# Performance work log

Measured on AMD Instinct MI355X. Metric: run time of the kernel, lower is better.

## Reference

```python
import jax, jax.numpy as jnp
import numpy as np

N_NODES = 50000
N_EDGES = 500000
IN_DIM = 128
HIDDEN = 32
HEADS = 8
OUT_DIM = HIDDEN * HEADS  # 256
NEG_SLOPE = 0.2


def setup_inputs() -> dict:
    key = jax.random.key(0)
    ks = jax.random.split(key, 10)
    s = lambda fan: 1.0 / np.sqrt(fan)
    x = jax.random.normal(ks[0], (N_NODES, IN_DIM), dtype=jnp.float32)
    edge_index = jax.random.randint(ks[1], (2, N_EDGES), 0, N_NODES, dtype=jnp.int32)
    W1 = jax.random.normal(ks[2], (IN_DIM, HEADS * HIDDEN), jnp.float32) * s(IN_DIM)
    a_src1 = jax.random.normal(ks[3], (HEADS, HIDDEN), jnp.float32) * s(HIDDEN)
    a_dst1 = jax.random.normal(ks[4], (HEADS, HIDDEN), jnp.float32) * s(HIDDEN)
    b1 = jnp.zeros((HEADS * HIDDEN,), jnp.float32)
    W2 = jax.random.normal(ks[5], (OUT_DIM, OUT_DIM), jnp.float32) * s(OUT_DIM)
    a_src2 = jax.random.normal(ks[6], (1, OUT_DIM), jnp.float32) * s(OUT_DIM)
    a_dst2 = jax.random.normal(ks[7], (1, OUT_DIM), jnp.float32) * s(OUT_DIM)
    b2 = jnp.zeros((OUT_DIM,), jnp.float32)
    return {"x": x, "edge_index": edge_index, "W1": W1, "a_src1": a_src1,
            "a_dst1": a_dst1, "b1": b1, "W2": W2, "a_src2": a_src2,
            "a_dst2": a_dst2, "b2": b2}


def _gat_layer(x, src, dst, W, a_src, a_dst, b, heads, ch, concat):
    N = x.shape[0]
    h = (x @ W).reshape(N, heads, ch)                      # [N,H,C]
    e_src = jnp.sum(h * a_src[None], axis=-1)              # [N,H]
    e_dst = jnp.sum(h * a_dst[None], axis=-1)              # [N,H]
    e = jax.nn.leaky_relu(e_src[src] + e_dst[dst], NEG_SLOPE)  # [E,H]
    # softmax over incoming edges of each destination node
    m = jax.ops.segment_max(e, dst, num_segments=N)        # [N,H]
    e = jnp.exp(e - m[dst])
    denom = jax.ops.segment_sum(e, dst, num_segments=N)    # [N,H]
    alpha = e / (denom[dst] + 1e-16)                       # [E,H]
    msg = h[src] * alpha[:, :, None]                       # [E,H,C]
    out = jax.ops.segment_sum(msg, dst, num_segments=N)    # [N,H,C]
    out = out.reshape(N, heads * ch) if concat else out.mean(axis=1)
    return out + b


def reference(x, edge_index, W1, a_src1, a_dst1, b1, W2, a_src2, a_dst2, b2):
    N = x.shape[0]
    # add self loops (PyG GATConv default)
    loops = jnp.arange(N, dtype=edge_index.dtype)
    src = jnp.concatenate([edge_index[0], loops])
    dst = jnp.concatenate([edge_index[1], loops])
    # dropout is identity in eval mode
    h = _gat_layer(x, src, dst, W1, a_src1, a_dst1, b1, HEADS, HIDDEN, True)
    h = jax.nn.elu(h)
    out = _gat_layer(h, src, dst, W2, a_src2, a_dst2, b2, 1, OUT_DIM, False)
    return out
```

## Files before the change

kernel.cpp:

```cpp
#include <hip/hip_runtime.h>
#include <math.h>

#define N_NODES 50000
#define E_ORIG  500000
#define E_TOT   550000
#define NB      196

typedef _Float16 half8 __attribute__((ext_vector_type(8)));
typedef _Float16 half4 __attribute__((ext_vector_type(4)));
typedef float    v4f   __attribute__((ext_vector_type(4)));

__global__ void k_prepw(const float* __restrict__ W1, const float* __restrict__ W2,
                        const float* __restrict__ as2, const float* __restrict__ ad2,
                        const int* __restrict__ ei,
                        _Float16* __restrict__ w1t, _Float16* __restrict__ w2t,
                        float* __restrict__ vs2, float* __restrict__ vd2,
                        int* __restrict__ deg) {
    int i = blockIdx.x * blockDim.x + threadIdx.x;
    if (i < E_TOT) {
        int d = (i < E_ORIG) ? ei[E_ORIG + i] : (i - E_ORIG);
        atomicAdd(&deg[d], 1);
        return;
    }
    int j = i - E_TOT;
    if (j < 128 * 256) {
        int k = j >> 8, c = j & 255;
        w1t[(size_t)c * 128 + k] = (_Float16)W1[j];
        return;
    }
    j -= 128 * 256;
    if (j < 256 * 256) {
        int k = j >> 8, c = j & 255;
        w2t[(size_t)c * 256 + k] = (_Float16)W2[j];
        return;
    }
    j -= 256 * 256;
    if (j < 256) {
        float s = 0.f, d = 0.f;
        for (int c = 0; c < 256; c++) {
            float w = W2[(size_t)j * 256 + c];
            s += w * as2[c];
            d += w * ad2[c];
        }
        vs2[j] = s;
        vd2[j] = d;
    }
}

__global__ __launch_bounds__(256) void k_blocksum(const int* __restrict__ deg,
                                                  int* __restrict__ bsum) {
    int t = threadIdx.x;
    int i = blockIdx.x * 256 + t;
    int v = (i < N_NODES) ? deg[i] : 0;
#pragma unroll
    for (int mk = 1; mk < 64; mk <<= 1) v += __shfl_xor(v, mk, 64);
    __shared__ int ws[4];
    if ((t & 63) == 0) ws[t >> 6] = v;
    __syncthreads();
    if (t == 0) bsum[blockIdx.x] = ws[0] + ws[1] + ws[2] + ws[3];
}

__global__ __launch_bounds__(256) void k_scanbsum(const int* __restrict__ bsum,
                                                  int* __restrict__ boff) {
    __shared__ int s[256];
    int t = threadIdx.x;
    int v = (t < NB) ? bsum[t] : 0;
    s[t] = v;
    __syncthreads();
    for (int o = 1; o < 256; o <<= 1) {
        int x = (t >= o) ? s[t - o] : 0;
        __syncthreads();
        s[t] += x;
        __syncthreads();
    }
    if (t <= NB) boff[t] = (t == 0) ? 0 : s[t - 1];
}

__global__ __launch_bounds__(256) void k_offsets(const int* __restrict__ deg,
                                                 const int* __restrict__ boff,
                                                 int* __restrict__ offsets,
                                                 int* __restrict__ cur) {
    __shared__ int s[256];
    int t = threadIdx.x;
    int i = blockIdx.x * 256 + t;
    int v = (i < N_NODES) ? deg[i] : 0;
    s[t] = v;
    __syncthreads();
    for (int o = 1; o < 256; o <<= 1) {
        int x = (t >= o) ? s[t - o] : 0;
        __syncthreads();
        s[t] += x;
        __syncthreads();
    }
    int off = boff[blockIdx.x] + s[t] - v;
    if (i <= N_NODES) {
        offsets[i] = off;
        if (i < N_NODES) cur[i] = off;
    }
}

__global__ void k_scatter(const int* __restrict__ ei, int* __restrict__ cur,
                          int* __restrict__ csr_src) {
    int e = blockIdx.x * blockDim.x + threadIdx.x;
    if (e >= E_TOT) return;
    int s, d;
    if (e < E_ORIG) { s = ei[e]; d = ei[E_ORIG + e]; }
    else            { s = e - E_ORIG; d = s; }
    int slot = atomicAdd(&cur[d], 1);
    csr_src[slot] = s;
}

__global__ __launch_bounds__(256) void k_gemm1(
    const float* __restrict__ X, const _Float16* __restrict__ Bt,
    const float* __restrict__ a_s, const float* __restrict__ a_d,
    _Float16* __restrict__ H, float* __restrict__ es, float* __restrict__ ed) {
    int t = threadIdx.x, w = t >> 6, lane = t & 63;
    int quad = lane >> 4, l16 = lane & 15;
    int row0 = blockIdx.x * 32;
    int colbase = w * 64;

    v4f acc[2][4];
#pragma unroll
    for (int i = 0; i < 2; i++)
#pragma unroll
        for (int j = 0; j < 4; j++) acc[i][j] = (v4f){0.f, 0.f, 0.f, 0.f};

    int r0 = row0 + l16;      if (r0 >= N_NODES) r0 = N_NODES - 1;
    int r1 = row0 + 16 + l16; if (r1 >= N_NODES) r1 = N_NODES - 1;
    const float4* a0p = (const float4*)(X + (size_t)r0 * 128) + quad * 2;
    const float4* a1p = (const float4*)(X + (size_t)r1 * 128) + quad * 2;
    const half8* bp[4];
#pragma unroll
    for (int ct = 0; ct < 4; ct++)
        bp[ct] = (const half8*)(Bt + (size_t)(colbase + ct * 16 + l16) * 128 + quad * 8);

#pragma unroll
    for (int kc = 0; kc < 4; kc++) {
        float4 f0 = a0p[kc * 8], f1 = a0p[kc * 8 + 1];
        float4 f2 = a1p[kc * 8], f3 = a1p[kc * 8 + 1];
        half8 av0 = (half8){(_Float16)f0.x, (_Float16)f0.y, (_Float16)f0.z, (_Float16)f0.w,
                            (_Float16)f1.x, (_Float16)f1.y, (_Float16)f1.z, (_Float16)f1.w};
        half8 av1 = (half8){(_Float16)f2.x, (_Float16)f2.y, (_Float16)f2.z, (_Float16)f2.w,
                            (_Float16)f3.x, (_Float16)f3.y, (_Float16)f3.z, (_Float16)f3.w};
#pragma unroll
        for (int ct = 0; ct < 4; ct++) {
            half8 bv = bp[ct][kc * 4];
            acc[0][ct] = __builtin_amdgcn_mfma_f32_16x16x32_f16(av0, bv, acc[0][ct], 0, 0, 0);
            acc[1][ct] = __builtin_amdgcn_mfma_f32_16x16x32_f16(av1, bv, acc[1][ct], 0, 0, 0);
        }
    }

    float asv[4], adv[4];
#pragma unroll
    for (int ct = 0; ct < 4; ct++) {
        asv[ct] = a_s[colbase + ct * 16 + l16];
        adv[ct] = a_d[colbase + ct * 16 + l16];
    }
#pragma unroll
    for (int rt = 0; rt < 2; rt++) {
#pragma unroll
        for (int hp = 0; hp < 2; hp++) {
#pragma unroll
            for (int reg = 0; reg < 4; reg++) {
                float ps = acc[rt][2 * hp][reg] * asv[2 * hp] +
                           acc[rt][2 * hp + 1][reg] * asv[2 * hp + 1];
                float pd = acc[rt][2 * hp][reg] * adv[2 * hp] +
                           acc[rt][2 * hp + 1][reg] * adv[2 * hp + 1];
#pragma unroll
                for (int mk = 1; mk < 16; mk <<= 1) {
                    ps += __shfl_xor(ps, mk, 64);
                    pd += __shfl_xor(pd, mk, 64);
                }
                if (l16 == 0) {
                    int row = row0 + rt * 16 + quad * 4 + reg;
                    if (row < N_NODES) {
                        int head = w * 2 + hp;
                        es[(size_t)row * 8 + head] = ps;
                        ed[(size_t)row * 8 + head] = pd;
                    }
                }
            }
        }
    }

    __shared__ _Float16 SH[16][264];
#pragma unroll
    for (int rt = 0; rt < 2; rt++) {
        if (rt) __syncthreads();
#pragma unroll
        for (int ct = 0; ct < 4; ct++)
#pragma unroll
            for (int reg = 0; reg < 4; reg++)
                SH[quad * 4 + reg][colbase + ct * 16 + l16] = (_Float16)acc[rt][ct][reg];
        __syncthreads();
#pragma unroll
        for (int j = 0; j < 2; j++) {
            int c = j * 256 + t;
            int row = c >> 5, col8 = c & 31;
            int gr = row0 + rt * 16 + row;
            if (gr < N_NODES)
                *(half8*)(H + (size_t)gr * 256 + col8 * 8) = *(const half8*)&SH[row][col8 * 8];
        }
    }
}

__global__ __launch_bounds__(256) void k_gemm2(
    const _Float16* __restrict__ A, const _Float16* __restrict__ Bt,
    const float* __restrict__ bias, float* __restrict__ OUT) {
    int t = threadIdx.x, w = t >> 6, lane = t & 63;
    int quad = lane >> 4, l16 = lane & 15;
    int row0 = blockIdx.x * 32;
    int colbase = w * 64;

    v4f acc[2][4];
#pragma unroll
    for (int i = 0; i < 2; i++)
#pragma unroll
        for (int j = 0; j < 4; j++) acc[i][j] = (v4f){0.f, 0.f, 0.f, 0.f};

    int r0 = row0 + l16;      if (r0 >= N_NODES) r0 = N_NODES - 1;
    int r1 = row0 + 16 + l16; if (r1 >= N_NODES) r1 = N_NODES - 1;
    const half8* a0 = (const half8*)(A + (size_t)r0 * 256 + quad * 8);
    const half8* a1 = (const half8*)(A + (size_t)r1 * 256 + quad * 8);
    const half8* bp[4];
#pragma unroll
    for (int ct = 0; ct < 4; ct++)
        bp[ct] = (const half8*)(Bt + (size_t)(colbase + ct * 16 + l16) * 256 + quad * 8);

#pragma unroll
    for (int kc = 0; kc < 8; kc++) {
        half8 av0 = a0[kc * 4];
        half8 av1 = a1[kc * 4];
#pragma unroll
        for (int ct = 0; ct < 4; ct++) {
            half8 bv = bp[ct][kc * 4];
            acc[0][ct] = __builtin_amdgcn_mfma_f32_16x16x32_f16(av0, bv, acc[0][ct], 0, 0, 0);
            acc[1][ct] = __builtin_amdgcn_mfma_f32_16x16x32_f16(av1, bv, acc[1][ct], 0, 0, 0);
        }
    }

    __shared__ float SF[16][260];
#pragma unroll
    for (int rt = 0; rt < 2; rt++) {
        if (rt) __syncthreads();
#pragma unroll
        for (int ct = 0; ct < 4; ct++)
#pragma unroll
            for (int reg = 0; reg < 4; reg++)
                SF[quad * 4 + reg][colbase + ct * 16 + l16] = acc[rt][ct][reg];
        __syncthreads();
#pragma unroll
        for (int j = 0; j < 4; j++) {
            int c = j * 256 + t;
            int row = c >> 6, c4 = c & 63;
            int gr = row0 + rt * 16 + row;
            if (gr < N_NODES) {
                float4 v = *(const float4*)&SF[row][c4 * 4];
                float4 bb = ((const float4*)bias)[c4];
                float4 o = make_float4(v.x + bb.x, v.y + bb.y, v.z + bb.z, v.w + bb.w);
                *(float4*)(OUT + (size_t)gr * 256 + c4 * 4) = o;
            }
        }
    }
}

#define EDGE1(I) {                                                         \
    unsigned su = (unsigned)__builtin_amdgcn_readlane(sreg, (I));          \
    float wb = wrow[(I)];                                                  \
    half4 hv = *((const half4*)((const char*)H1 + ((size_t)su << 9)) + lane); \
    a0 += wb * (float)hv[0]; a1 += wb * (float)hv[1];                      \
    a2 += wb * (float)hv[2]; a3 += wb * (float)hv[3];                      \
    den += wb; }

__global__ __launch_bounds__(256) void k_agg1(
    const _Float16* __restrict__ H1, const float* __restrict__ es,
    const float* __restrict__ ed, const int* __restrict__ offsets,
    const int* __restrict__ csr_src, const float* __restrict__ b1,
    const float* __restrict__ vs2, const float* __restrict__ vd2,
    _Float16* __restrict__ out1, float* __restrict__ es2,
    float* __restrict__ ed2) {
    int t = threadIdx.x, w = t >> 6, lane = t & 63;
    int n = blockIdx.x * 4 + w;
    int hB = lane >> 3;
    int beg = offsets[n];
    int deg = offsets[n + 1] - beg;

    float edv[8];
    {
        const float4* edp = (const float4*)(ed + (size_t)n * 8);
        float4 d0 = edp[0], d1 = edp[1];
        edv[0] = d0.x; edv[1] = d0.y; edv[2] = d0.z; edv[3] = d0.w;
        edv[4] = d1.x; edv[5] = d1.y; edv[6] = d1.z; edv[7] = d1.w;
    }

    __shared__ float WT[4][8][68];
    float* wrow = &WT[w][hB][0];

    float a0 = 0.f, a1 = 0.f, a2 = 0.f, a3 = 0.f, den = 0.f;

    for (int base = 0; base < deg; base += 64) {
        int rem = deg - base; if (rem > 64) rem = 64;
        int idx = beg + base + lane;
        if (idx >= E_TOT) idx = E_TOT - 1;
        int sreg = csr_src[idx];

        {
            const float4* ep = (const float4*)(es + ((size_t)(unsigned)sreg << 3));
            float4 e0 = ep[0], e1 = ep[1];
            float l0 = e0.x + edv[0], l1 = e0.y + edv[1];
            float l2 = e0.z + edv[2], l3 = e0.w + edv[3];
            float l4 = e1.x + edv[4], l5 = e1.y + edv[5];
            float l6 = e1.z + edv[6], l7 = e1.w + edv[7];
            l0 = fmaxf(l0, 0.2f * l0); l1 = fmaxf(l1, 0.2f * l1);
            l2 = fmaxf(l2, 0.2f * l2); l3 = fmaxf(l3, 0.2f * l3);
            l4 = fmaxf(l4, 0.2f * l4); l5 = fmaxf(l5, 0.2f * l5);
            l6 = fmaxf(l6, 0.2f * l6); l7 = fmaxf(l7, 0.2f * l7);
            WT[w][0][lane] = __expf(l0); WT[w][1][lane] = __expf(l1);
            WT[w][2][lane] = __expf(l2); WT[w][3][lane] = __expf(l3);
            WT[w][4][lane] = __expf(l4); WT[w][5][lane] = __expf(l5);
            WT[w][6][lane] = __expf(l6); WT[w][7][lane] = __expf(l7);
        }
        asm volatile("s_waitcnt lgkmcnt(0)" ::: "memory");

        int i = 0, nf = rem & ~7;
        for (; i < nf; i += 8) {
            EDGE1(i);     EDGE1(i + 1); EDGE1(i + 2); EDGE1(i + 3);
            EDGE1(i + 4); EDGE1(i + 5); EDGE1(i + 6); EDGE1(i + 7);
        }
        if (rem & 4) { EDGE1(i); EDGE1(i + 1); EDGE1(i + 2); EDGE1(i + 3); i += 4; }
        if (rem & 2) { EDGE1(i); EDGE1(i + 1); i += 2; }
        if (rem & 1) { EDGE1(i); }
    }

    float r = 1.f / (den + 1e-16f);
    float4 bb = ((const float4*)b1)[lane];
    float o0 = a0 * r + bb.x, o1 = a1 * r + bb.y;
    float o2 = a2 * r + bb.z, o3 = a3 * r + bb.w;
    o0 = o0 > 0.f ? o0 : __expf(o0) - 1.f;
    o1 = o1 > 0.f ? o1 : __expf(o1) - 1.f;
    o2 = o2 > 0.f ? o2 : __expf(o2) - 1.f;
    o3 = o3 > 0.f ? o3 : __expf(o3) - 1.f;
    ((half4*)(out1 + (size_t)n * 256))[lane] =
        (half4){(_Float16)o0, (_Float16)o1, (_Float16)o2, (_Float16)o3};

    float4 vs = ((const float4*)vs2)[lane];
    float4 vd = ((const float4*)vd2)[lane];
    float ps = o0 * vs.x + o1 * vs.y + o2 * vs.z + o3 * vs.w;
    float pd = o0 * vd.x + o1 * vd.y + o2 * vd.z + o3 * vd.w;
#pragma unroll
    for (int mk = 1; mk < 64; mk <<= 1) {
        ps += __shfl_xor(ps, mk, 64);
        pd += __shfl_xor(pd, mk, 64);
    }
    if (lane == 0) { es2[n] = ps; ed2[n] = pd; }
}

#define EDGE2(I) {                                                         \
    unsigned su = (unsigned)__builtin_amdgcn_readlane(sreg, (I));          \
    float wb = __int_as_float(__builtin_amdgcn_readlane(wbits, (I)));      \
    half4 hv = *((const half4*)((const char*)O1 + ((size_t)su << 9)) + lane); \
    a0 += wb * (float)hv[0]; a1 += wb * (float)hv[1];                      \
    a2 += wb * (float)hv[2]; a3 += wb * (float)hv[3];                      \
    den += wb; }

__global__ __launch_bounds__(256) void k_agg2(
    const _Float16* __restrict__ O1, const float* __restrict__ es2,
    const float* __restrict__ ed2, const int* __restrict__ offsets,
    const int* __restrict__ csr_src, _Float16* __restrict__ xagg) {
    int t = threadIdx.x, w = t >> 6, lane = t & 63;
    int n = blockIdx.x * 4 + w;
    int beg = offsets[n];
    int deg = offsets[n + 1] - beg;
    float edn = ed2[n];

    float a0 = 0.f, a1 = 0.f, a2 = 0.f, a3 = 0.f, den = 0.f;

    for (int base = 0; base < deg; base += 64) {
        int rem = deg - base; if (rem > 64) rem = 64;
        int idx = beg + base + lane;
        if (idx >= E_TOT) idx = E_TOT - 1;
        int sreg = csr_src[idx];

        float l = es2[sreg] + edn;
        l = fmaxf(l, 0.2f * l);
        int wbits = __float_as_int(__expf(l));

        int i = 0, nf = rem & ~7;
        for (; i < nf; i += 8) {
            EDGE2(i);     EDGE2(i + 1); EDGE2(i + 2); EDGE2(i + 3);
            EDGE2(i + 4); EDGE2(i + 5); EDGE2(i + 6); EDGE2(i + 7);
        }
        if (rem & 4) { EDGE2(i); EDGE2(i + 1); EDGE2(i + 2); EDGE2(i + 3); i += 4; }
        if (rem & 2) { EDGE2(i); EDGE2(i + 1); i += 2; }
        if (rem & 1) { EDGE2(i); }
    }

    float r = 1.f / (den + 1e-16f);
    ((half4*)(xagg + (size_t)n * 256))[lane] =
        (half4){(_Float16)(a0 * r), (_Float16)(a1 * r),
                (_Float16)(a2 * r), (_Float16)(a3 * r)};
}

extern "C" void kernel_launch(void* const* d_in, const int* in_sizes, int n_in,
                              void* d_out, int out_size, void* d_ws, size_t ws_size,
                              hipStream_t stream) {
    const float* x   = (const float*)d_in[0];
    const int*   ei  = (const int*)d_in[1];
    const float* W1  = (const float*)d_in[2];
    const float* as1 = (const float*)d_in[3];
    const float* ad1 = (const float*)d_in[4];
    const float* b1  = (const float*)d_in[5];
    const float* W2  = (const float*)d_in[6];
    const float* as2 = (const float*)d_in[7];
    const float* ad2 = (const float*)d_in[8];
    const float* b2  = (const float*)d_in[9];
    float* out = (float*)d_out;

    char* ws = (char*)d_ws;
    size_t off = 0;
    auto alloc = [&](size_t bytes) {
        void* p = ws + off;
        off = (off + bytes + 255) & ~(size_t)255;
        return p;
    };
    _Float16* h1h     = (_Float16*)alloc((size_t)N_NODES * 256 * 2);
    _Float16* out1h   = (_Float16*)alloc((size_t)N_NODES * 256 * 2);
    _Float16* xagg    = (_Float16*)alloc((size_t)N_NODES * 256 * 2);
    _Float16* w1t     = (_Float16*)alloc((size_t)128 * 256 * 2);
    _Float16* w2t     = (_Float16*)alloc((size_t)256 * 256 * 2);
    float*    es1     = (float*)alloc((size_t)N_NODES * 8 * 4);
    float*    ed1     = (float*)alloc((size_t)N_NODES * 8 * 4);
    float*    es2     = (float*)alloc((size_t)N_NODES * 4);
    float*    ed2     = (float*)alloc((size_t)N_NODES * 4);
    float*    vs2     = (float*)alloc(256 * 4);
    float*    vd2     = (float*)alloc(256 * 4);
    int*      deg     = (int*)alloc((size_t)N_NODES * 4);
    int*      offsets = (int*)alloc((size_t)(N_NODES + 1) * 4);
    int*      cur     = (int*)alloc((size_t)N_NODES * 4);
    int*      csr_src = (int*)alloc((size_t)E_TOT * 4);
    int*      bsum    = (int*)alloc((size_t)NB * 4);
    int*      boff    = (int*)alloc((size_t)(NB + 1) * 4);

    const int TB = 256;
    int gridE = (E_TOT + TB - 1) / TB;
    int gridG = (N_NODES + 31) / 32;
    int gridA = N_NODES / 4;

    hipMemsetAsync(deg, 0, (size_t)N_NODES * 4, stream);
    int prepN = E_TOT + 128 * 256 + 256 * 256 + 256;
    k_prepw<<<(prepN + TB - 1) / TB, TB, 0, stream>>>(W1, W2, as2, ad2, ei,
                                                      w1t, w2t, vs2, vd2, deg);
    k_blocksum<<<NB, TB, 0, stream>>>(deg, bsum);
    k_scanbsum<<<1, TB, 0, stream>>>(bsum, boff);
    k_offsets<<<NB, TB, 0, stream>>>(deg, boff, offsets, cur);
    k_scatter<<<gridE, TB, 0, stream>>>(ei, cur, csr_src);

    k_gemm1<<<gridG, TB, 0, stream>>>(x, w1t, as1, ad1, h1h, es1, ed1);
    k_agg1<<<gridA, TB, 0, stream>>>(h1h, es1, ed1, offsets, csr_src, b1,
                                     vs2, vd2, out1h, es2, ed2);

    k_agg2<<<gridA, TB, 0, stream>>>(out1h, es2, ed2, offsets, csr_src, xagg);
    k_gemm2<<<gridG, TB, 0, stream>>>(xagg, w2t, b2, out);
}
```

Before: 327.8 us.

## Store features head-major and aggregate per head with edge-parallel lanes

H1, es/ed, and out1 now use a head-major layout, so each aggregation block works on one head's 32-channel slice. The slice per node is 64 bytes, meant to keep the gathered working set per head cache-resident. Inside a wave, 8 edges are processed in parallel, each by 4 lanes loading half8, and the partial sums are reduced with shuffles. The layer-2 attention logits are now built with atomicAdd across heads, which needs extra memsets and gives up deterministic float summation order. Agg2 reads O1 per head but still writes xagg row-major.

```diff
diff --git a/kernel.cpp b/kernel.cpp
--- a/kernel.cpp
+++ b/kernel.cpp
@@ -5,6 +5,7 @@
 #define E_ORIG  500000
 #define E_TOT   550000
 #define NB      196
+#define AGG_G   1568
 
 typedef _Float16 half8 __attribute__((ext_vector_type(8)));
 typedef _Float16 half4 __attribute__((ext_vector_type(4)));
@@ -175,8 +176,8 @@
                     int row = row0 + rt * 16 + quad * 4 + reg;
                     if (row < N_NODES) {
                         int head = w * 2 + hp;
-                        es[(size_t)row * 8 + head] = ps;
-                        ed[(size_t)row * 8 + head] = pd;
+                        es[(size_t)head * N_NODES + row] = ps;
+                        ed[(size_t)head * N_NODES + row] = pd;
                     }
                 }
             }
@@ -198,8 +199,11 @@
             int c = j * 256 + t;
             int row = c >> 5, col8 = c & 31;
             int gr = row0 + rt * 16 + row;
-            if (gr < N_NODES)
-                *(half8*)(H + (size_t)gr * 256 + col8 * 8) = *(const half8*)&SH[row][col8 * 8];
+            if (gr < N_NODES) {
+                int head = col8 >> 2, sub = col8 & 3;
+                *(half8*)(H + ((size_t)head * N_NODES + gr) * 32 + sub * 8) =
+                    *(const half8*)&SH[row][col8 * 8];
+            }
         }
     }
 }
@@ -264,141 +268,130 @@
     }
 }
 
-#define EDGE1(I) {                                                         \
-    unsigned su = (unsigned)__builtin_amdgcn_readlane(sreg, (I));          \
-    float wb = wrow[(I)];                                                  \
-    half4 hv = *((const half4*)((const char*)H1 + ((size_t)su << 9)) + lane); \
-    a0 += wb * (float)hv[0]; a1 += wb * (float)hv[1];                      \
-    a2 += wb * (float)hv[2]; a3 += wb * (float)hv[3];                      \
-    den += wb; }
-
 __global__ __launch_bounds__(256) void k_agg1(
-    const _Float16* __restrict__ H1, const float* __restrict__ es,
-    const float* __restrict__ ed, const int* __restrict__ offsets,
+    const _Float16* __restrict__ Hs, const float* __restrict__ esh,
+    const float* __restrict__ edh, const int* __restrict__ offsets,
     const int* __restrict__ csr_src, const float* __restrict__ b1,
     const float* __restrict__ vs2, const float* __restrict__ vd2,
-    _Float16* __restrict__ out1, float* __restrict__ es2,
+    _Float16* __restrict__ out1s, float* __restrict__ es2,
     float* __restrict__ ed2) {
     int t = threadIdx.x, w = t >> 6, lane = t & 63;
-    int n = blockIdx.x * 4 + w;
-    int hB = lane >> 3;
-    int beg = offsets[n];
-    int deg = offsets[n + 1] - beg;
-
-    float edv[8];
-    {
-        const float4* edp = (const float4*)(ed + (size_t)n * 8);
-        float4 d0 = edp[0], d1 = edp[1];
-        edv[0] = d0.x; edv[1] = d0.y; edv[2] = d0.z; edv[3] = d0.w;
-        edv[4] = d1.x; edv[5] = d1.y; edv[6] = d1.z; edv[7] = d1.w;
-    }
-
-    __shared__ float WT[4][8][68];
-    float* wrow = &WT[w][hB][0];
-
-    float a0 = 0.f, a1 = 0.f, a2 = 0.f, a3 = 0.f, den = 0.f;
-
-    for (int base = 0; base < deg; base += 64) {
-        int rem = deg - base; if (rem > 64) rem = 64;
-        int idx = beg + base + lane;
-        if (idx >= E_TOT) idx = E_TOT - 1;
-        int sreg = csr_src[idx];
-
-        {
-            const float4* ep = (const float4*)(es + ((size_t)(unsigned)sreg << 3));
-            float4 e0 = ep[0], e1 = ep[1];
-            float l0 = e0.x + edv[0], l1 = e0.y + edv[1];
-            float l2 = e0.z + edv[2], l3 = e0.w + edv[3];
-            float l4 = e1.x + edv[4], l5 = e1.y + edv[5];
-            float l6 = e1.z + edv[6], l7 = e1.w + edv[7];
-            l0 = fmaxf(l0, 0.2f * l0); l1 = fmaxf(l1, 0.2f * l1);
-            l2 = fmaxf(l2, 0.2f * l2); l3 = fmaxf(l3, 0.2f * l3);
-            l4 = fmaxf(l4, 0.2f * l4); l5 = fmaxf(l5, 0.2f * l5);
-            l6 = fmaxf(l6, 0.2f * l6); l7 = fmaxf(l7, 0.2f * l7);
-            WT[w][0][lane] = __expf(l0); WT[w][1][lane] = __expf(l1);
-            WT[w][2][lane] = __expf(l2); WT[w][3][lane] = __expf(l3);
-            WT[w][4][lane] = __expf(l4); WT[w][5][lane] = __expf(l5);
-            WT[w][6][lane] = __expf(l6); WT[w][7][lane] = __expf(l7);
-        }
-        asm volatile("s_waitcnt lgkmcnt(0)" ::: "memory");
-
-        int i = 0, nf = rem & ~7;
-        for (; i < nf; i += 8) {
-            EDGE1(i);     EDGE1(i + 1); EDGE1(i + 2); EDGE1(i + 3);
-            EDGE1(i + 4); EDGE1(i + 5); EDGE1(i + 6); EDGE1(i + 7);
-        }
-        if (rem & 4) { EDGE1(i); EDGE1(i + 1); EDGE1(i + 2); EDGE1(i + 3); i += 4; }
-        if (rem & 2) { EDGE1(i); EDGE1(i + 1); i += 2; }
-        if (rem & 1) { EDGE1(i); }
-    }
-
-    float r = 1.f / (den + 1e-16f);
-    float4 bb = ((const float4*)b1)[lane];
-    float o0 = a0 * r + bb.x, o1 = a1 * r + bb.y;
-    float o2 = a2 * r + bb.z, o3 = a3 * r + bb.w;
-    o0 = o0 > 0.f ? o0 : __expf(o0) - 1.f;
-    o1 = o1 > 0.f ? o1 : __expf(o1) - 1.f;
-    o2 = o2 > 0.f ? o2 : __expf(o2) - 1.f;
-    o3 = o3 > 0.f ? o3 : __expf(o3) - 1.f;
-    ((half4*)(out1 + (size_t)n * 256))[lane] =
-        (half4){(_Float16)o0, (_Float16)o1, (_Float16)o2, (_Float16)o3};
-
-    float4 vs = ((const float4*)vs2)[lane];
-    float4 vd = ((const float4*)vd2)[lane];
-    float ps = o0 * vs.x + o1 * vs.y + o2 * vs.z + o3 * vs.w;
-    float pd = o0 * vd.x + o1 * vd.y + o2 * vd.z + o3 * vd.w;
-#pragma unroll
-    for (int mk = 1; mk < 64; mk <<= 1) {
-        ps += __shfl_xor(ps, mk, 64);
-        pd += __shfl_xor(pd, mk, 64);
-    }
-    if (lane == 0) { es2[n] = ps; ed2[n] = pd; }
-}
-
-#define EDGE2(I) {                                                         \
-    unsigned su = (unsigned)__builtin_amdgcn_readlane(sreg, (I));          \
-    float wb = __int_as_float(__builtin_amdgcn_readlane(wbits, (I)));      \
-    half4 hv = *((const half4*)((const char*)O1 + ((size_t)su << 9)) + lane); \
-    a0 += wb * (float)hv[0]; a1 += wb * (float)hv[1];                      \
-    a2 += wb * (float)hv[2]; a3 += wb * (float)hv[3];                      \
-    den += wb; }
+    int h = blockIdx.x & 7;
+    int gb = blockIdx.x >> 3;
+    int half = lane >> 5;
+    int slot = (lane >> 2) & 7;
+    int oct  = lane & 3;
+
+    const _Float16* Hb  = Hs  + (size_t)h * N_NODES * 32;
+    const float*    esb = esh + (size_t)h * N_NODES;
+    const float*    edb = edh + (size_t)h * N_NODES;
+
+    float bj[8], vsj[8], vdj[8];
+#pragma unroll
+    for (int j = 0; j < 8; j++) {
+        int c = h * 32 + oct * 8 + j;
+        bj[j] = b1[c]; vsj[j] = vs2[c]; vdj[j] = vd2[c];
+    }
+
+    int stride = AGG_G * 4 * 2;
+    for (int n0 = (gb * 4 + w) * 2; n0 < N_NODES; n0 += stride) {
+        int n = n0 + half;
+        int beg = offsets[n];
+        int deg = offsets[n + 1] - beg;
+        float edn = edb[n];
+
+        float a[8] = {0.f, 0.f, 0.f, 0.f, 0.f, 0.f, 0.f, 0.f};
+        float den = 0.f;
+        for (int base = 0; base < deg; base += 8) {
+            int off = base + slot;
+            int idx = beg + (off < deg ? off : deg - 1);
+            int s = csr_src[idx];
+            float l = esb[s] + edn;
+            l = fmaxf(l, 0.2f * l);
+            float wt = (off < deg) ? __expf(l) : 0.f;
+            half8 hv = *(const half8*)(Hb + (size_t)s * 32 + oct * 8);
+#pragma unroll
+            for (int j = 0; j < 8; j++) a[j] += wt * (float)hv[j];
+            den += wt;
+        }
+#pragma unroll
+        for (int mk = 4; mk <= 16; mk <<= 1) {
+#pragma unroll
+            for (int j = 0; j < 8; j++) a[j] += __shfl_xor(a[j], mk, 64);
+            den += __shfl_xor(den, mk, 64);
+        }
+
+        float r = 1.f / (den + 1e-16f);
+        half8 ov;
+        float ps = 0.f, pd = 0.f;
+#pragma unroll
+        for (int j = 0; j < 8; j++) {
+            float v = a[j] * r + bj[j];
+            v = v > 0.f ? v : __expf(v) - 1.f;
+            ov[j] = (_Float16)v;
+            ps += v * vsj[j];
+            pd += v * vdj[j];
+        }
+        if (slot == 0)
+            *(half8*)(out1s + ((size_t)h * N_NODES + n) * 32 + oct * 8) = ov;
+
+        ps += __shfl_xor(ps, 1, 64); ps += __shfl_xor(ps, 2, 64);
+        pd += __shfl_xor(pd, 1, 64); pd += __shfl_xor(pd, 2, 64);
+        if ((lane & 31) == 0) {
+            atomicAdd(&es2[n], ps);
+            atomicAdd(&ed2[n], pd);
+        }
+    }
+}
 
 __global__ __launch_bounds__(256) void k_agg2(
-    const _Float16* __restrict__ O1, const float* __restrict__ es2,
+    const _Float16* __restrict__ O1s, const float* __restrict__ es2,
     const float* __restrict__ ed2, const int* __restrict__ offsets,
     const int* __restrict__ csr_src, _Float16* __restrict__ xagg) {
     int t = threadIdx.x, w = t >> 6, lane = t & 63;
-    int n = blockIdx.x * 4 + w;
-    int beg = offsets[n];
-    int deg = offsets[n + 1] - beg;
-    float edn = ed2[n];
-
-    float a0 = 0.f, a1 = 0.f, a2 = 0.f, a3 = 0.f, den = 0.f;
-
-    for (int base = 0; base < deg; base += 64) {
-        int rem = deg - base; if (rem > 64) rem = 64;
-        int idx = beg + base + lane;
-        if (idx >= E_TOT) idx = E_TOT - 1;
-        int sreg = csr_src[idx];
-
-        float l = es2[sreg] + edn;
-        l = fmaxf(l, 0.2f * l);
-        int wbits = __float_as_int(__expf(l));
-
-        int i = 0, nf = rem & ~7;
-        for (; i < nf; i += 8) {
-            EDGE2(i);     EDGE2(i + 1); EDGE2(i + 2); EDGE2(i + 3);
-            EDGE2(i + 4); EDGE2(i + 5); EDGE2(i + 6); EDGE2(i + 7);
-        }
-        if (rem & 4) { EDGE2(i); EDGE2(i + 1); EDGE2(i + 2); EDGE2(i + 3); i += 4; }
-        if (rem & 2) { EDGE2(i); EDGE2(i + 1); i += 2; }
-        if (rem & 1) { EDGE2(i); }
-    }
-
-    float r = 1.f / (den + 1e-16f);
-    ((half4*)(xagg + (size_t)n * 256))[lane] =
-        (half4){(_Float16)(a0 * r), (_Float16)(a1 * r),
-                (_Float16)(a2 * r), (_Float16)(a3 * r)};
+    int h = blockIdx.x & 7;
+    int gb = blockIdx.x >> 3;
+    int half = lane >> 5;
+    int slot = (lane >> 2) & 7;
+    int oct  = lane & 3;
+
+    const _Float16* Ob = O1s + (size_t)h * N_NODES * 32;
+
+    int stride = AGG_G * 4 * 2;
+    for (int n0 = (gb * 4 + w) * 2; n0 < N_NODES; n0 += stride) {
+        int n = n0 + half;
+        int beg = offsets[n];
+        int deg = offsets[n + 1] - beg;
+        float edn = ed2[n];
+
+        float a[8] = {0.f, 0.f, 0.f, 0.f, 0.f, 0.f, 0.f, 0.f};
+        float den = 0.f;
+        for (int base = 0; base < deg; base += 8) {
+            int off = base + slot;
+            int idx = beg + (off < deg ? off : deg - 1);
+            int s = csr_src[idx];
+            float l = es2[s] + edn;
+            l = fmaxf(l, 0.2f * l);
+            float wt = (off < deg) ? __expf(l) : 0.f;
+            half8 hv = *(const half8*)(Ob + (size_t)s * 32 + oct * 8);
+#pragma unroll
+            for (int j = 0; j < 8; j++) a[j] += wt * (float)hv[j];
+            den += wt;
+        }
+#pragma unroll
+        for (int mk = 4; mk <= 16; mk <<= 1) {
+#pragma unroll
+            for (int j = 0; j < 8; j++) a[j] += __shfl_xor(a[j], mk, 64);
+            den += __shfl_xor(den, mk, 64);
+        }
+
+        float r = 1.f / (den + 1e-16f);
+        half8 ov;
+#pragma unroll
+        for (int j = 0; j < 8; j++) ov[j] = (_Float16)(a[j] * r);
+        if (slot == 0)
+            *(half8*)(xagg + (size_t)n * 256 + h * 32 + oct * 8) = ov;
+    }
 }
 
 extern "C" void kernel_launch(void* const* d_in, const int* in_sizes, int n_in,
@@ -444,9 +437,11 @@
     const int TB = 256;
     int gridE = (E_TOT + TB - 1) / TB;
     int gridG = (N_NODES + 31) / 32;
-    int gridA = N_NODES / 4;
+    int gridA = AGG_G * 8;
 
     hipMemsetAsync(deg, 0, (size_t)N_NODES * 4, stream);
+    hipMemsetAsync(es2, 0, (size_t)N_NODES * 4, stream);
+    hipMemsetAsync(ed2, 0, (size_t)N_NODES * 4, stream);
     int prepN = E_TOT + 128 * 256 + 256 * 256 + 256;
     k_prepw<<<(prepN + TB - 1) / TB, TB, 0, stream>>>(W1, W2, as2, ad2, ei,
                                                       w1t, w2t, vs2, vd2, deg);
```

New measurement: 400.6 us. 22.2% more time.
